# Optimization experiments

Measured on AMD Instinct MI355X. Metric: run time of the kernel, lower is better.

## Reference

```python
import jax, jax.numpy as jnp
import numpy as np
from jax import lax

NUM_POINTS = 1024  # num_points from __init__
BIG = jnp.float32(1e10)


def setup_inputs() -> dict:
    key = jax.random.key(0)
    B, N = 8, 131072
    points = jax.random.normal(key, (B, N, 3), dtype=jnp.float32)
    return {"points": points}


def furthest_point_sampling(points, m):
    """points: [B, N, 3] -> indices [B, m] (int32).
    Standard FPS: start at index 0, iteratively pick the point farthest
    from the current selected set, maintaining a running min-distance.
    """
    B, N, _ = points.shape

    def body(carry, _):
        min_dist, last_idx = carry  # [B, N], [B]
        last_pt = jnp.take_along_axis(points, last_idx[:, None, None], axis=1)  # [B,1,3]
        d = jnp.sum((points - last_pt) ** 2, axis=-1)  # [B, N]
        min_dist = jnp.minimum(min_dist, d)
        nxt = jnp.argmax(min_dist, axis=-1).astype(jnp.int32)  # [B]
        return (min_dist, nxt), nxt

    init_idx = jnp.zeros((B,), dtype=jnp.int32)
    init_dist = jnp.full((B, N), BIG, dtype=points.dtype)
    _, rest = lax.scan(body, (init_dist, init_idx), None, length=m - 1)  # [m-1, B]
    idx = jnp.concatenate([init_idx[None, :], rest], axis=0)  # [m, B]
    return idx.T  # [B, m]


def reference(points):
    idx = furthest_point_sampling(points, NUM_POINTS)            # [B, m]
    xyz1 = jnp.take_along_axis(points, idx[:, :, None], axis=1)  # [B, m, 3]
    return (idx, xyz1)
```

## Files before the change

### kernel.cpp

```cpp
#include <hip/hip_runtime.h>
#include <stdint.h>


#define BATCHES 8
#define NPTS    131072
#define MSEL    1024
#define NBLK    32
#define CHUNK   (NPTS / NBLK)
#define NTH     256
#define PPT     (CHUNK / NTH)
#define NWAVE   (NTH / 64)
#define L2_TIMEOUT_ROUNDS 2000

typedef unsigned int       u32;
typedef unsigned long long u64;
typedef u32 u32x4 __attribute__((ext_vector_type(4)));
typedef u32 u32x2 __attribute__((ext_vector_type(2)));

__device__ __forceinline__ void l2_store_slot(void* p, u32x4 a, u32x2 b) {
    asm volatile("global_store_dwordx4 %0, %1, off sc0\n\t"
                 "global_store_dwordx2 %2, %3, off sc0"
                 :: "v"((u32*)p), "v"(a), "v"(((u32*)p) + 4), "v"(b)
                 : "memory");
}
__device__ __forceinline__ void l2_load_slot(const void* p, u32x4& a, u32x2& b) {
    u32x4 ra; u32x2 rb;
    asm volatile("global_load_dwordx4 %0, %2, off sc0\n\t"
                 "global_load_dwordx2 %1, %3, off sc0\n\t"
                 "s_waitcnt vmcnt(0)"
                 : "=&v"(ra), "=&v"(rb)
                 : "v"((const u32*)p), "v"(((const u32*)p) + 4)
                 : "memory");
    a = ra; b = rb;
}

__global__ __launch_bounds__(NTH, 1) void fps_kernel(
    const float* __restrict__ pts,
    float* __restrict__ out,
    char* __restrict__ l2base,
    u64*  __restrict__ icslots,
    int pad)
{
    __shared__ float lx[CHUNK];
    __shared__ float ly[CHUNK];
    __shared__ float lz[CHUNK];
    __shared__ u64 wkey[NWAVE];
    __shared__ float curs[4];

    const int bid   = blockIdx.x;
    const int b     = bid & (BATCHES - 1);
    const int blk   = bid / BATCHES;
    const int tid   = threadIdx.x;
    const int gbase = blk * CHUNK;
    const float* bp = pts + (size_t)b * NPTS * 3;

    float px[PPT], py[PPT], pz[PPT], md[PPT];
    #pragma unroll
    for (int k = 0; k < PPT; ++k) {
        const int j = k * NTH + tid;
        const size_t gi = (size_t)(gbase + j) * 3;
        px[k] = bp[gi + 0];
        py[k] = bp[gi + 1];
        pz[k] = bp[gi + 2];
        md[k] = 1e10f;
        lx[j] = px[k]; ly[j] = py[k]; lz[j] = pz[k];
    }
    const u32 relt = (u32)(NPTS - 1) - (u32)(gbase + tid);

    float cx = bp[0], cy = bp[1], cz = bp[2];
    if (blk == 0 && tid == 0) {
        out[b * MSEL] = 0.0f;
        float* oxyz = out + BATCHES * MSEL;
        oxyz[(size_t)(b * MSEL) * 3 + 0] = cx;
        oxyz[(size_t)(b * MSEL) * 3 + 1] = cy;
        oxyz[(size_t)(b * MSEL) * 3 + 2] = cz;
    }
    __syncthreads();

    const int wv = tid >> 6;
    const int ln = tid & 63;
    bool useAgent = false;

    for (int s = 1; s < MSEL; ++s) {
        u64 bk = 0ull;
        #pragma unroll
        for (int k = 0; k < PPT; ++k) {
            float dx = __fsub_rn(px[k], cx);
            float dy = __fsub_rn(py[k], cy);
            float dz = __fsub_rn(pz[k], cz);
            float d  = __fadd_rn(__fadd_rn(__fmul_rn(dx, dx), __fmul_rn(dy, dy)),
                                 __fmul_rn(dz, dz));
            float nm = fminf(md[k], d);
            md[k] = nm;
            u64 key = ((u64)__float_as_uint(nm) << 17)
                    | (u64)(relt - (u32)(k * NTH));
            bk = (bk > key) ? bk : key;
        }
        #pragma unroll
        for (int o = 32; o > 0; o >>= 1) {
            u64 t = __shfl_xor(bk, o, 64);
            bk = (bk > t) ? bk : t;
        }
        if (ln == 0) wkey[wv] = bk;
        __syncthreads();

        const u32 tag = (u32)s;
        char* base = l2base + ((size_t)(s & 1) * BATCHES + b) * NBLK * (size_t)pad;
        const size_t icb = ((size_t)(s & 1) * BATCHES + b) * NBLK;

        if (wv == 1 && ln == 0) {
            u64 k0 = wkey[0];
            #pragma unroll
            for (int w = 1; w < NWAVE; ++w) k0 = (k0 > wkey[w]) ? k0 : wkey[w];
            const u64 sv = ((k0 >> 17) << 27) | ((k0 & 0x1FFFFull) << 10) | tag;
            __hip_atomic_store(&icslots[icb + blk], sv,
                               __ATOMIC_RELAXED, __HIP_MEMORY_SCOPE_AGENT);
        }

        if (wv == 0) {
            if (ln == 0) {
                u64 k0 = wkey[0];
                #pragma unroll
                for (int w = 1; w < NWAVE; ++w) k0 = (k0 > wkey[w]) ? k0 : wkey[w];
                const u32 rel = (u32)(k0 & 0x1FFFFull);
                const u32 db  = (u32)(k0 >> 17);
                const int j   = (int)((u32)(NPTS - 1) - rel) - gbase;
                u32x4 a; u32x2 bg;
                a.x = db; a.y = (rel << 10) | tag;
                a.z = __float_as_uint(lx[j]); a.w = __float_as_uint(ly[j]);
                bg.x = __float_as_uint(lz[j]); bg.y = tag;
                l2_store_slot(base + (size_t)blk * pad, a, bg);
            }
            u64 k = 0ull; float x = 0.f, y = 0.f, z = 0.f;
            if (!useAgent) {
                u32x4 A; u32x2 Bv; bool done = false;
                int r = 0;
                for (;;) {
                    if (ln < NBLK && !done) {
                        l2_load_slot(base + (size_t)ln * pad, A, Bv);
                        done = ((A.y & 1023u) == tag) & (Bv.y == tag);
                    }
                    if (__all((ln >= NBLK) | done)) break;
                    if (++r >= L2_TIMEOUT_ROUNDS) { useAgent = true; break; }
                    __builtin_amdgcn_s_sleep(1);
                }
                if (!useAgent && ln < NBLK) {
                    k = ((u64)A.x << 17) | (u64)(A.y >> 10);
                    x = __uint_as_float(A.z);
                    y = __uint_as_float(A.w);
                    z = __uint_as_float(Bv.x);
                }
            }
            if (useAgent) {
                u64 ak = 0ull;
                for (;;) {
                    if (ln < NBLK)
                        ak = __hip_atomic_load(&icslots[icb + ln],
                                               __ATOMIC_RELAXED,
                                               __HIP_MEMORY_SCOPE_AGENT);
                    if (__all((ln >= NBLK) | ((u32)(ak & 1023ull) == tag)))
                        break;
                    __builtin_amdgcn_s_sleep(1);
                }
                #pragma unroll
                for (int o = 16; o > 0; o >>= 1) {
                    u64 t = __shfl_xor(ak, o, 64);
                    ak = (ak > t) ? ak : t;
                }
                const u32 widx = (u32)(NPTS - 1) - (u32)((ak >> 10) & 0x1FFFFull);
                if (ln < 3) {
                    const float v = bp[(size_t)widx * 3 + ln];
                    curs[ln] = v;
                    if (blk == 0)
                        out[BATCHES * MSEL + (size_t)(b * MSEL + s) * 3 + ln] = v;
                }
                if (ln == 0 && blk == 0) out[b * MSEL + s] = (float)widx;
            } else {
                #pragma unroll
                for (int o = 16; o > 0; o >>= 1) {
                    u64 kk = __shfl_xor(k, o, 64);
                    float xx = __shfl_xor(x, o, 64);
                    float yy = __shfl_xor(y, o, 64);
                    float zz = __shfl_xor(z, o, 64);
                    const bool p = kk > k;
                    k = p ? kk : k;
                    x = p ? xx : x;
                    y = p ? yy : y;
                    z = p ? zz : z;
                }
                if (ln == 0) {
                    const u32 widx = (u32)(NPTS - 1) - (u32)(k & 0x1FFFFull);
                    curs[0] = x; curs[1] = y; curs[2] = z;
                    if (blk == 0) {
                        out[b * MSEL + s] = (float)widx;
                        float* oxyz = out + BATCHES * MSEL;
                        oxyz[(size_t)(b * MSEL + s) * 3 + 0] = x;
                        oxyz[(size_t)(b * MSEL + s) * 3 + 1] = y;
                        oxyz[(size_t)(b * MSEL + s) * 3 + 2] = z;
                    }
                }
            }
        }
        __syncthreads();
        cx = curs[0]; cy = curs[1]; cz = curs[2];
    }
}

extern "C" void kernel_launch(void* const* d_in, const int* in_sizes, int n_in,
                              void* d_out, int out_size, void* d_ws, size_t ws_size,
                              hipStream_t stream) {
    const float* pts = (const float*)d_in[0];
    float* out = (float*)d_out;

    const int pad = (ws_size >= (size_t)(2 * BATCHES * NBLK * 128 + 4096))
                        ? 128 : 32;
    char* l2base = (char*)d_ws;
    u64* icslots = (u64*)((char*)d_ws + (size_t)2 * BATCHES * NBLK * pad);

    fps_kernel<<<dim3(BATCHES * NBLK), dim3(NTH), 0, stream>>>(
        pts, out, l2base, icslots, pad);
}
```

Before: 2.249 ms.

## Replace per-block slot polling with atomic max key and arrival counter

Result: slower. 4.664 ms (+107.3%).

```diff
diff --git a/kernel.cpp b/kernel.cpp
--- a/kernel.cpp
+++ b/kernel.cpp
@@ -10,40 +10,19 @@
 #define NTH     256
 #define PPT     (CHUNK / NTH)
 #define NWAVE   (NTH / 64)
-#define L2_TIMEOUT_ROUNDS 2000
+#define L2_TIMEOUT_ROUNDS 4000
 
 typedef unsigned int       u32;
 typedef unsigned long long u64;
 typedef u32 u32x4 __attribute__((ext_vector_type(4)));
-typedef u32 u32x2 __attribute__((ext_vector_type(2)));
-
-__device__ __forceinline__ void l2_store_slot(void* p, u32x4 a, u32x2 b) {
-    asm volatile("global_store_dwordx4 %0, %1, off sc0\n\t"
-                 "global_store_dwordx2 %2, %3, off sc0"
-                 :: "v"((u32*)p), "v"(a), "v"(((u32*)p) + 4), "v"(b)
-                 : "memory");
-}
-__device__ __forceinline__ void l2_load_slot(const void* p, u32x4& a, u32x2& b) {
-    u32x4 ra; u32x2 rb;
-    asm volatile("global_load_dwordx4 %0, %2, off sc0\n\t"
-                 "global_load_dwordx2 %1, %3, off sc0\n\t"
-                 "s_waitcnt vmcnt(0)"
-                 : "=&v"(ra), "=&v"(rb)
-                 : "v"((const u32*)p), "v"(((const u32*)p) + 4)
-                 : "memory");
-    a = ra; b = rb;
-}
 
 __global__ __launch_bounds__(NTH, 1) void fps_kernel(
     const float* __restrict__ pts,
     float* __restrict__ out,
-    char* __restrict__ l2base,
-    u64*  __restrict__ icslots,
+    char* __restrict__ ws,
     int pad)
 {
-    __shared__ float lx[CHUNK];
-    __shared__ float ly[CHUNK];
-    __shared__ float lz[CHUNK];
+    __shared__ float lx[CHUNK], ly[CHUNK], lz[CHUNK];
     __shared__ u64 wkey[NWAVE];
     __shared__ float curs[4];
 
@@ -53,6 +32,11 @@
     const int tid   = threadIdx.x;
     const int gbase = blk * CHUNK;
     const float* bp = pts + (size_t)b * NPTS * 3;
+
+    char* ctl  = ws + (size_t)b * 512;
+    u32*  cntp = (u32*)(ctl + 256);
+    char* plb0 = ws + 4096;
+    u64*  ic   = (u64*)(ws + 4096 + (size_t)2 * BATCHES * NBLK * pad);
 
     float px[PPT], py[PPT], pz[PPT], md[PPT];
     #pragma unroll
@@ -105,91 +89,80 @@
         __syncthreads();
 
         const u32 tag = (u32)s;
-        char* base = l2base + ((size_t)(s & 1) * BATCHES + b) * NBLK * (size_t)pad;
-        const size_t icb = ((size_t)(s & 1) * BATCHES + b) * NBLK;
+        const int par = s & 1;
+        u64*  keyp   = (u64*)(ctl + par * 128);
+        char* plbase = plb0 + ((size_t)(par * BATCHES + b) * NBLK) * pad;
+        const size_t icb = (size_t)(par * BATCHES + b) * NBLK;
 
         if (wv == 1 && ln == 0) {
             u64 k0 = wkey[0];
             #pragma unroll
             for (int w = 1; w < NWAVE; ++w) k0 = (k0 > wkey[w]) ? k0 : wkey[w];
-            const u64 sv = ((k0 >> 17) << 27) | ((k0 & 0x1FFFFull) << 10) | tag;
-            __hip_atomic_store(&icslots[icb + blk], sv,
+            const u32 rel = (u32)(k0 & 0x1FFFFull);
+            const int j = (int)((u32)(NPTS - 1) - rel) - gbase;
+            u32x4 pl;
+            pl.x = __float_as_uint(lx[j]);
+            pl.y = __float_as_uint(ly[j]);
+            pl.z = __float_as_uint(lz[j]);
+            pl.w = tag;
+            const u64 akey = ((u64)tag << 49) | k0;
+            asm volatile(
+                "global_store_dwordx4 %0, %1, off sc0\n\t"
+                "global_atomic_umax_x2 %2, %3, off\n\t"
+                "s_waitcnt vmcnt(0)\n\t"
+                "global_atomic_add %4, %5, off"
+                :: "v"(plbase + (size_t)blk * pad), "v"(pl),
+                   "v"(keyp), "v"(akey),
+                   "v"(cntp), "v"(1u)
+                : "memory");
+            const u64 sv = ((k0 >> 17) << 27) | ((u64)rel << 10) | (u64)tag;
+            __hip_atomic_store(&ic[icb + blk], sv,
                                __ATOMIC_RELAXED, __HIP_MEMORY_SCOPE_AGENT);
         }
 
         if (wv == 0) {
-            if (ln == 0) {
-                u64 k0 = wkey[0];
-                #pragma unroll
-                for (int w = 1; w < NWAVE; ++w) k0 = (k0 > wkey[w]) ? k0 : wkey[w];
-                const u32 rel = (u32)(k0 & 0x1FFFFull);
-                const u32 db  = (u32)(k0 >> 17);
-                const int j   = (int)((u32)(NPTS - 1) - rel) - gbase;
-                u32x4 a; u32x2 bg;
-                a.x = db; a.y = (rel << 10) | tag;
-                a.z = __float_as_uint(lx[j]); a.w = __float_as_uint(ly[j]);
-                bg.x = __float_as_uint(lz[j]); bg.y = tag;
-                l2_store_slot(base + (size_t)blk * pad, a, bg);
+            bool det = false;
+            u32 widx = 0; float x = 0.f, y = 0.f, z = 0.f;
+            if (!useAgent) {
+                const u32 target = 32u * tag;
+                int r = 0; u32 c;
+                for (;;) {
+                    asm volatile("global_load_dword %0, %1, off sc0\n\t"
+                                 "s_waitcnt vmcnt(0)"
+                                 : "=v"(c) : "v"(cntp) : "memory");
+                    if (c >= target) { det = true; break; }
+                    if (++r >= L2_TIMEOUT_ROUNDS) { useAgent = true; break; }
+                    if (r > 16) __builtin_amdgcn_s_sleep(1);
+                }
             }
-            u64 k = 0ull; float x = 0.f, y = 0.f, z = 0.f;
-            if (!useAgent) {
-                u32x4 A; u32x2 Bv; bool done = false;
-                int r = 0;
-                for (;;) {
-                    if (ln < NBLK && !done) {
-                        l2_load_slot(base + (size_t)ln * pad, A, Bv);
-                        done = ((A.y & 1023u) == tag) & (Bv.y == tag);
-                    }
-                    if (__all((ln >= NBLK) | done)) break;
-                    if (++r >= L2_TIMEOUT_ROUNDS) { useAgent = true; break; }
-                    __builtin_amdgcn_s_sleep(1);
-                }
-                if (!useAgent && ln < NBLK) {
-                    k = ((u64)A.x << 17) | (u64)(A.y >> 10);
-                    x = __uint_as_float(A.z);
-                    y = __uint_as_float(A.w);
-                    z = __uint_as_float(Bv.x);
+            if (det) {
+                u64 kf = 0ull; u32x4 PL = {0, 0, 0, 0};
+                if (ln < 32) {
+                    const char* plp = plbase + (size_t)ln * pad;
+                    asm volatile(
+                        "global_load_dwordx2 %0, %2, off sc0\n\t"
+                        "global_load_dwordx4 %1, %3, off sc0\n\t"
+                        "s_waitcnt vmcnt(0)"
+                        : "=&v"(kf), "=&v"(PL)
+                        : "v"(keyp), "v"(plp)
+                        : "memory");
+                }
+                const u32 klo  = (u32)__shfl((int)(u32)kf, 0, 64);
+                const u32 khi  = (u32)__shfl((int)(u32)(kf >> 32), 0, 64);
+                const u32 ktag = khi >> 17;
+                const u32 rel  = klo & 0x1FFFFu;
+                widx = (u32)(NPTS - 1) - rel;
+                const int wblk = (int)(widx >> 12);
+                x = __shfl(__uint_as_float(PL.x), wblk, 64);
+                y = __shfl(__uint_as_float(PL.y), wblk, 64);
+                z = __shfl(__uint_as_float(PL.z), wblk, 64);
+                const u32 wtag = (u32)__shfl((int)PL.w, wblk, 64);
+                if (ktag != tag || wtag != tag) {
+                    det = false; useAgent = true;
                 }
             }
-            if (useAgent) {
-                u64 ak = 0ull;
-                for (;;) {
-                    if (ln < NBLK)
-                        ak = __hip_atomic_load(&icslots[icb + ln],
-                                               __ATOMIC_RELAXED,
-                                               __HIP_MEMORY_SCOPE_AGENT);
-                    if (__all((ln >= NBLK) | ((u32)(ak & 1023ull) == tag)))
-                        break;
-                    __builtin_amdgcn_s_sleep(1);
-                }
-                #pragma unroll
-                for (int o = 16; o > 0; o >>= 1) {
-                    u64 t = __shfl_xor(ak, o, 64);
-                    ak = (ak > t) ? ak : t;
-                }
-                const u32 widx = (u32)(NPTS - 1) - (u32)((ak >> 10) & 0x1FFFFull);
-                if (ln < 3) {
-                    const float v = bp[(size_t)widx * 3 + ln];
-                    curs[ln] = v;
-                    if (blk == 0)
-                        out[BATCHES * MSEL + (size_t)(b * MSEL + s) * 3 + ln] = v;
-                }
-                if (ln == 0 && blk == 0) out[b * MSEL + s] = (float)widx;
-            } else {
-                #pragma unroll
-                for (int o = 16; o > 0; o >>= 1) {
-                    u64 kk = __shfl_xor(k, o, 64);
-                    float xx = __shfl_xor(x, o, 64);
-                    float yy = __shfl_xor(y, o, 64);
-                    float zz = __shfl_xor(z, o, 64);
-                    const bool p = kk > k;
-                    k = p ? kk : k;
-                    x = p ? xx : x;
-                    y = p ? yy : y;
-                    z = p ? zz : z;
-                }
+            if (det) {
                 if (ln == 0) {
-                    const u32 widx = (u32)(NPTS - 1) - (u32)(k & 0x1FFFFull);
                     curs[0] = x; curs[1] = y; curs[2] = z;
                     if (blk == 0) {
                         out[b * MSEL + s] = (float)widx;
@@ -199,6 +172,31 @@
                         oxyz[(size_t)(b * MSEL + s) * 3 + 2] = z;
                     }
                 }
+            } else {
+                u64 ak = 0ull;
+                for (;;) {
+                    if (ln < NBLK)
+                        ak = __hip_atomic_load(&ic[icb + ln], __ATOMIC_RELAXED,
+                                               __HIP_MEMORY_SCOPE_AGENT);
+                    if (__all((ln >= NBLK) | ((u32)(ak & 1023ull) ==
+                                              (tag & 1023u))))
+                        break;
+                    __builtin_amdgcn_s_sleep(1);
+                }
+                #pragma unroll
+                for (int o = 16; o > 0; o >>= 1) {
+                    u64 t = __shfl_xor(ak, o, 64);
+                    ak = (ak > t) ? ak : t;
+                }
+                const u32 fwidx =
+                    (u32)(NPTS - 1) - (u32)((ak >> 10) & 0x1FFFFull);
+                if (ln < 3) {
+                    const float v = bp[(size_t)fwidx * 3 + ln];
+                    curs[ln] = v;
+                    if (blk == 0)
+                        out[BATCHES * MSEL + (size_t)(b * MSEL + s) * 3 + ln] = v;
+                }
+                if (ln == 0 && blk == 0) out[b * MSEL + s] = (float)fwidx;
             }
         }
         __syncthreads();
@@ -212,11 +210,10 @@
     const float* pts = (const float*)d_in[0];
     float* out = (float*)d_out;
 
-    const int pad = (ws_size >= (size_t)(2 * BATCHES * NBLK * 128 + 4096))
+    const int pad = (ws_size >= (size_t)(4096 + 2 * BATCHES * NBLK * 128 + 4096))
                         ? 128 : 32;
-    char* l2base = (char*)d_ws;
-    u64* icslots = (u64*)((char*)d_ws + (size_t)2 * BATCHES * NBLK * pad);
+    hipMemsetAsync(d_ws, 0, 4096, stream);
 
     fps_kernel<<<dim3(BATCHES * NBLK), dim3(NTH), 0, stream>>>(
-        pts, out, l2base, icslots, pad);
+        pts, out, (char*)d_ws, pad);
 }
```

## Speculatively select two FPS points per grid-wide sync round via top-2 reduction

Applied to the files above, without the earlier changes.

Measured after the change: 3.861 ms. 71.6% more time.

```diff
diff --git a/kernel.cpp b/kernel.cpp
--- a/kernel.cpp
+++ b/kernel.cpp
@@ -10,20 +10,28 @@
 #define NTH     256
 #define PPT     (CHUNK / NTH)
 #define NWAVE   (NTH / 64)
-#define L2_TIMEOUT_ROUNDS 2000
+#define L2_TIMEOUT_ROUNDS 4000
 
 typedef unsigned int       u32;
 typedef unsigned long long u64;
 typedef u32 u32x4 __attribute__((ext_vector_type(4)));
 typedef u32 u32x2 __attribute__((ext_vector_type(2)));
 
-__device__ __forceinline__ void l2_store_slot(void* p, u32x4 a, u32x2 b) {
+__device__ __forceinline__ void pmerge(u64& a1, u64& a2, u64 b1, u64 b2) {
+    const u64 lo = (a1 < b1) ? a1 : b1;
+    const u64 hi = (a1 < b1) ? b1 : a1;
+    const u64 m2 = (a2 > b2) ? a2 : b2;
+    a1 = hi;
+    a2 = (lo > m2) ? lo : m2;
+}
+
+__device__ __forceinline__ void st_slot(void* p, u32x4 a, u32x2 b) {
     asm volatile("global_store_dwordx4 %0, %1, off sc0\n\t"
                  "global_store_dwordx2 %2, %3, off sc0"
                  :: "v"((u32*)p), "v"(a), "v"(((u32*)p) + 4), "v"(b)
                  : "memory");
 }
-__device__ __forceinline__ void l2_load_slot(const void* p, u32x4& a, u32x2& b) {
+__device__ __forceinline__ void ld_slot(const void* p, u32x4& a, u32x2& b) {
     u32x4 ra; u32x2 rb;
     asm volatile("global_load_dwordx4 %0, %2, off sc0\n\t"
                  "global_load_dwordx2 %1, %3, off sc0\n\t"
@@ -37,15 +45,12 @@
 __global__ __launch_bounds__(NTH, 1) void fps_kernel(
     const float* __restrict__ pts,
     float* __restrict__ out,
-    char* __restrict__ l2base,
-    u64*  __restrict__ icslots,
+    char* __restrict__ ws,
     int pad)
 {
-    __shared__ float lx[CHUNK];
-    __shared__ float ly[CHUNK];
-    __shared__ float lz[CHUNK];
-    __shared__ u64 wkey[NWAVE];
-    __shared__ float curs[4];
+    __shared__ float lx[CHUNK], ly[CHUNK], lz[CHUNK];
+    __shared__ u64 wkey[NWAVE][2];
+    __shared__ float curs[8];
 
     const int bid   = blockIdx.x;
     const int b     = bid & (BATCHES - 1);
@@ -53,6 +58,9 @@
     const int tid   = threadIdx.x;
     const int gbase = blk * CHUNK;
     const float* bp = pts + (size_t)b * NPTS * 3;
+
+    char* plb0 = ws;
+    u64*  ic   = (u64*)(ws + (size_t)2 * BATCHES * 64 * pad);
 
     float px[PPT], py[PPT], pz[PPT], md[PPT];
     #pragma unroll
@@ -67,142 +75,232 @@
     }
     const u32 relt = (u32)(NPTS - 1) - (u32)(gbase + tid);
 
-    float cx = bp[0], cy = bp[1], cz = bp[2];
+    float c1x = bp[0], c1y = bp[1], c1z = bp[2];
+    float c2x = c1x, c2y = c1y, c2z = c1z;
+    bool have2 = false;
     if (blk == 0 && tid == 0) {
         out[b * MSEL] = 0.0f;
         float* oxyz = out + BATCHES * MSEL;
-        oxyz[(size_t)(b * MSEL) * 3 + 0] = cx;
-        oxyz[(size_t)(b * MSEL) * 3 + 1] = cy;
-        oxyz[(size_t)(b * MSEL) * 3 + 2] = cz;
+        oxyz[(size_t)(b * MSEL) * 3 + 0] = c1x;
+        oxyz[(size_t)(b * MSEL) * 3 + 1] = c1y;
+        oxyz[(size_t)(b * MSEL) * 3 + 2] = c1z;
     }
     __syncthreads();
 
     const int wv = tid >> 6;
     const int ln = tid & 63;
     bool useAgent = false;
-
-    for (int s = 1; s < MSEL; ++s) {
-        u64 bk = 0ull;
-        #pragma unroll
-        for (int k = 0; k < PPT; ++k) {
-            float dx = __fsub_rn(px[k], cx);
-            float dy = __fsub_rn(py[k], cy);
-            float dz = __fsub_rn(pz[k], cz);
-            float d  = __fadd_rn(__fadd_rn(__fmul_rn(dx, dx), __fmul_rn(dy, dy)),
-                                 __fmul_rn(dz, dz));
-            float nm = fminf(md[k], d);
-            md[k] = nm;
-            u64 key = ((u64)__float_as_uint(nm) << 17)
-                    | (u64)(relt - (u32)(k * NTH));
-            bk = (bk > key) ? bk : key;
+    int s = 1;
+
+    for (int rc = 1; s < MSEL; ++rc) {
+        u64 a1 = 0ull, a2 = 0ull;
+        if (have2) {
+            #pragma unroll
+            for (int k = 0; k < PPT; ++k) {
+                float dx = __fsub_rn(px[k], c1x);
+                float dy = __fsub_rn(py[k], c1y);
+                float dz = __fsub_rn(pz[k], c1z);
+                float d1 = __fadd_rn(__fadd_rn(__fmul_rn(dx, dx),
+                                               __fmul_rn(dy, dy)),
+                                     __fmul_rn(dz, dz));
+                float ex = __fsub_rn(px[k], c2x);
+                float ey = __fsub_rn(py[k], c2y);
+                float ez = __fsub_rn(pz[k], c2z);
+                float d2 = __fadd_rn(__fadd_rn(__fmul_rn(ex, ex),
+                                               __fmul_rn(ey, ey)),
+                                     __fmul_rn(ez, ez));
+                float nm = fminf(fminf(md[k], d1), d2);
+                md[k] = nm;
+                u64 key = ((u64)__float_as_uint(nm) << 17)
+                        | (u64)(relt - (u32)(k * NTH));
+                const bool gt = key > a1;
+                const u64 mx2 = (key > a2) ? key : a2;
+                a2 = gt ? a1 : mx2;
+                a1 = gt ? key : a1;
+            }
+        } else {
+            #pragma unroll
+            for (int k = 0; k < PPT; ++k) {
+                float dx = __fsub_rn(px[k], c1x);
+                float dy = __fsub_rn(py[k], c1y);
+                float dz = __fsub_rn(pz[k], c1z);
+                float d1 = __fadd_rn(__fadd_rn(__fmul_rn(dx, dx),
+                                               __fmul_rn(dy, dy)),
+                                     __fmul_rn(dz, dz));
+                float nm = fminf(md[k], d1);
+                md[k] = nm;
+                u64 key = ((u64)__float_as_uint(nm) << 17)
+                        | (u64)(relt - (u32)(k * NTH));
+                const bool gt = key > a1;
+                const u64 mx2 = (key > a2) ? key : a2;
+                a2 = gt ? a1 : mx2;
+                a1 = gt ? key : a1;
+            }
         }
         #pragma unroll
         for (int o = 32; o > 0; o >>= 1) {
-            u64 t = __shfl_xor(bk, o, 64);
-            bk = (bk > t) ? bk : t;
+            u64 b1 = __shfl_xor(a1, o, 64);
+            u64 b2 = __shfl_xor(a2, o, 64);
+            pmerge(a1, a2, b1, b2);
         }
-        if (ln == 0) wkey[wv] = bk;
+        if (ln == 0) { wkey[wv][0] = a1; wkey[wv][1] = a2; }
         __syncthreads();
 
-        const u32 tag = (u32)s;
-        char* base = l2base + ((size_t)(s & 1) * BATCHES + b) * NBLK * (size_t)pad;
-        const size_t icb = ((size_t)(s & 1) * BATCHES + b) * NBLK;
+        const u32 tag = (u32)rc;
+        const int par = rc & 1;
+        char* plbase = plb0 + ((size_t)(par * BATCHES + b) * 64) * pad;
+        const size_t icb = (size_t)(par * BATCHES + b) * 64;
 
         if (wv == 1 && ln == 0) {
-            u64 k0 = wkey[0];
+            u64 k1 = wkey[0][0], k2 = wkey[0][1];
             #pragma unroll
-            for (int w = 1; w < NWAVE; ++w) k0 = (k0 > wkey[w]) ? k0 : wkey[w];
-            const u64 sv = ((k0 >> 17) << 27) | ((k0 & 0x1FFFFull) << 10) | tag;
-            __hip_atomic_store(&icslots[icb + blk], sv,
+            for (int w = 1; w < NWAVE; ++w) pmerge(k1, k2, wkey[w][0], wkey[w][1]);
+            const u32 rel1 = (u32)(k1 & 0x1FFFFull);
+            const u32 rel2 = (u32)(k2 & 0x1FFFFull);
+            const int j1 = (int)((u32)(NPTS - 1) - rel1) - gbase;
+            const int j2 = (int)((u32)(NPTS - 1) - rel2) - gbase;
+            u32x4 A; u32x2 Bv;
+            A.x = (u32)(k1 >> 17); A.y = (rel1 << 10) | tag;
+            A.z = __float_as_uint(lx[j1]); A.w = __float_as_uint(ly[j1]);
+            Bv.x = __float_as_uint(lz[j1]); Bv.y = tag;
+            st_slot(plbase + (size_t)blk * pad, A, Bv);
+            A.x = (u32)(k2 >> 17); A.y = (rel2 << 10) | tag;
+            A.z = __float_as_uint(lx[j2]); A.w = __float_as_uint(ly[j2]);
+            Bv.x = __float_as_uint(lz[j2]); Bv.y = tag;
+            st_slot(plbase + (size_t)(32 + blk) * pad, A, Bv);
+            __hip_atomic_store(&ic[icb + 2 * blk],
+                               ((k1 >> 17) << 27) | ((u64)rel1 << 10) | tag,
+                               __ATOMIC_RELAXED, __HIP_MEMORY_SCOPE_AGENT);
+            __hip_atomic_store(&ic[icb + 2 * blk + 1],
+                               ((k2 >> 17) << 27) | ((u64)rel2 << 10) | tag,
                                __ATOMIC_RELAXED, __HIP_MEMORY_SCOPE_AGENT);
         }
 
         if (wv == 0) {
-            if (ln == 0) {
-                u64 k0 = wkey[0];
-                #pragma unroll
-                for (int w = 1; w < NWAVE; ++w) k0 = (k0 > wkey[w]) ? k0 : wkey[w];
-                const u32 rel = (u32)(k0 & 0x1FFFFull);
-                const u32 db  = (u32)(k0 >> 17);
-                const int j   = (int)((u32)(NPTS - 1) - rel) - gbase;
-                u32x4 a; u32x2 bg;
-                a.x = db; a.y = (rel << 10) | tag;
-                a.z = __float_as_uint(lx[j]); a.w = __float_as_uint(ly[j]);
-                bg.x = __float_as_uint(lz[j]); bg.y = tag;
-                l2_store_slot(base + (size_t)blk * pad, a, bg);
-            }
-            u64 k = 0ull; float x = 0.f, y = 0.f, z = 0.f;
+            u32x4 LA = {0, 0, 0, 0}; u32x2 LB = {0, 0};
+            bool done = false;
             if (!useAgent) {
-                u32x4 A; u32x2 Bv; bool done = false;
+                const char* myp = plbase + (size_t)ln * pad;
                 int r = 0;
                 for (;;) {
-                    if (ln < NBLK && !done) {
-                        l2_load_slot(base + (size_t)ln * pad, A, Bv);
-                        done = ((A.y & 1023u) == tag) & (Bv.y == tag);
+                    if (!done) {
+                        u32x4 ta; u32x2 tb;
+                        ld_slot(myp, ta, tb);
+                        if (((ta.y & 1023u) == tag) & (tb.y == tag)) {
+                            LA = ta; LB = tb; done = true;
+                        }
                     }
-                    if (__all((ln >= NBLK) | done)) break;
+                    if (__all(done)) break;
                     if (++r >= L2_TIMEOUT_ROUNDS) { useAgent = true; break; }
+                    if (r > 16) __builtin_amdgcn_s_sleep(1);
+                }
+            }
+            if (!useAgent) {
+                u64 k1 = ((u64)LA.x << 17) | (u64)(LA.y >> 10);
+                u64 k2 = 0ull;
+                #pragma unroll
+                for (int o = 32; o > 0; o >>= 1) {
+                    u64 b1 = __shfl_xor(k1, o, 64);
+                    u64 b2 = __shfl_xor(k2, o, 64);
+                    pmerge(k1, k2, b1, b2);
+                }
+                const u32 rel1  = (u32)(k1 & 0x1FFFFull);
+                const u32 rel2  = (u32)(k2 & 0x1FFFFull);
+                const u32 widx1 = (u32)(NPTS - 1) - rel1;
+                const u32 widx2 = (u32)(NPTS - 1) - rel2;
+                const int wb1   = (int)(widx1 >> 12);
+                const int wbb   = (int)(widx2 >> 12);
+                const int src2  = (wbb == wb1) ? (32 + wb1) : wbb;
+                const float x1 = __shfl(__uint_as_float(LA.z), wb1, 64);
+                const float y1 = __shfl(__uint_as_float(LA.w), wb1, 64);
+                const float z1 = __shfl(__uint_as_float(LB.x), wb1, 64);
+                const float x2 = __shfl(__uint_as_float(LA.z), src2, 64);
+                const float y2 = __shfl(__uint_as_float(LA.w), src2, 64);
+                const float z2 = __shfl(__uint_as_float(LB.x), src2, 64);
+                const float ddx = __fsub_rn(x2, x1);
+                const float ddy = __fsub_rn(y2, y1);
+                const float ddz = __fsub_rn(z2, z1);
+                const float dd  = __fadd_rn(__fadd_rn(__fmul_rn(ddx, ddx),
+                                                      __fmul_rn(ddy, ddy)),
+                                            __fmul_rn(ddz, ddz));
+                const bool spec = (__float_as_uint(dd) >= (u32)(k2 >> 17))
+                                  && (s + 1 < MSEL);
+                if (ln == 0) {
+                    curs[0] = x1; curs[1] = y1; curs[2] = z1;
+                    curs[3] = x2; curs[4] = y2; curs[5] = z2;
+                    curs[6] = spec ? 1.0f : 0.0f;
+                    if (blk == 0) {
+                        out[b * MSEL + s] = (float)widx1;
+                        float* oxyz = out + BATCHES * MSEL;
+                        oxyz[(size_t)(b * MSEL + s) * 3 + 0] = x1;
+                        oxyz[(size_t)(b * MSEL + s) * 3 + 1] = y1;
+                        oxyz[(size_t)(b * MSEL + s) * 3 + 2] = z1;
+                        if (spec) {
+                            out[b * MSEL + s + 1] = (float)widx2;
+                            oxyz[(size_t)(b * MSEL + s + 1) * 3 + 0] = x2;
+                            oxyz[(size_t)(b * MSEL + s + 1) * 3 + 1] = y2;
+                            oxyz[(size_t)(b * MSEL + s + 1) * 3 + 2] = z2;
+                        }
+                    }
+                }
+            } else {
+                const int ii = (ln < 32) ? (2 * ln) : (2 * (ln - 32) + 1);
+                u64 sv = 0ull;
+                for (;;) {
+                    sv = __hip_atomic_load(&ic[icb + ii], __ATOMIC_RELAXED,
+                                           __HIP_MEMORY_SCOPE_AGENT);
+                    if (__all((u32)(sv & 1023ull) == (tag & 1023u))) break;
                     __builtin_amdgcn_s_sleep(1);
                 }
-                if (!useAgent && ln < NBLK) {
-                    k = ((u64)A.x << 17) | (u64)(A.y >> 10);
-                    x = __uint_as_float(A.z);
-                    y = __uint_as_float(A.w);
-                    z = __uint_as_float(Bv.x);
-                }
-            }
-            if (useAgent) {
-                u64 ak = 0ull;
-                for (;;) {
-                    if (ln < NBLK)
-                        ak = __hip_atomic_load(&icslots[icb + ln],
-                                               __ATOMIC_RELAXED,
-                                               __HIP_MEMORY_SCOPE_AGENT);
-                    if (__all((ln >= NBLK) | ((u32)(ak & 1023ull) == tag)))
-                        break;
-                    __builtin_amdgcn_s_sleep(1);
-                }
+                u64 k1 = ((sv >> 27) << 17) | ((sv >> 10) & 0x1FFFFull);
+                u64 k2 = 0ull;
                 #pragma unroll
-                for (int o = 16; o > 0; o >>= 1) {
-                    u64 t = __shfl_xor(ak, o, 64);
-                    ak = (ak > t) ? ak : t;
-                }
-                const u32 widx = (u32)(NPTS - 1) - (u32)((ak >> 10) & 0x1FFFFull);
-                if (ln < 3) {
-                    const float v = bp[(size_t)widx * 3 + ln];
-                    curs[ln] = v;
-                    if (blk == 0)
-                        out[BATCHES * MSEL + (size_t)(b * MSEL + s) * 3 + ln] = v;
-                }
-                if (ln == 0 && blk == 0) out[b * MSEL + s] = (float)widx;
-            } else {
-                #pragma unroll
-                for (int o = 16; o > 0; o >>= 1) {
-                    u64 kk = __shfl_xor(k, o, 64);
-                    float xx = __shfl_xor(x, o, 64);
-                    float yy = __shfl_xor(y, o, 64);
-                    float zz = __shfl_xor(z, o, 64);
-                    const bool p = kk > k;
-                    k = p ? kk : k;
-                    x = p ? xx : x;
-                    y = p ? yy : y;
-                    z = p ? zz : z;
-                }
+                for (int o = 32; o > 0; o >>= 1) {
+                    u64 b1 = __shfl_xor(k1, o, 64);
+                    u64 b2 = __shfl_xor(k2, o, 64);
+                    pmerge(k1, k2, b1, b2);
+                }
+                const u32 widx1 = (u32)(NPTS - 1) - (u32)(k1 & 0x1FFFFull);
+                const u32 widx2 = (u32)(NPTS - 1) - (u32)(k2 & 0x1FFFFull);
                 if (ln == 0) {
-                    const u32 widx = (u32)(NPTS - 1) - (u32)(k & 0x1FFFFull);
-                    curs[0] = x; curs[1] = y; curs[2] = z;
+                    const float x1 = bp[(size_t)widx1 * 3 + 0];
+                    const float y1 = bp[(size_t)widx1 * 3 + 1];
+                    const float z1 = bp[(size_t)widx1 * 3 + 2];
+                    const float x2 = bp[(size_t)widx2 * 3 + 0];
+                    const float y2 = bp[(size_t)widx2 * 3 + 1];
+                    const float z2 = bp[(size_t)widx2 * 3 + 2];
+                    const float ddx = __fsub_rn(x2, x1);
+                    const float ddy = __fsub_rn(y2, y1);
+                    const float ddz = __fsub_rn(z2, z1);
+                    const float dd  = __fadd_rn(__fadd_rn(__fmul_rn(ddx, ddx),
+                                                          __fmul_rn(ddy, ddy)),
+                                                __fmul_rn(ddz, ddz));
+                    const bool spec = (__float_as_uint(dd) >= (u32)(k2 >> 17))
+                                      && (s + 1 < MSEL);
+                    curs[0] = x1; curs[1] = y1; curs[2] = z1;
+                    curs[3] = x2; curs[4] = y2; curs[5] = z2;
+                    curs[6] = spec ? 1.0f : 0.0f;
                     if (blk == 0) {
-                        out[b * MSEL + s] = (float)widx;
+                        out[b * MSEL + s] = (float)widx1;
                         float* oxyz = out + BATCHES * MSEL;
-                        oxyz[(size_t)(b * MSEL + s) * 3 + 0] = x;
-                        oxyz[(size_t)(b * MSEL + s) * 3 + 1] = y;
-                        oxyz[(size_t)(b * MSEL + s) * 3 + 2] = z;
+                        oxyz[(size_t)(b * MSEL + s) * 3 + 0] = x1;
+                        oxyz[(size_t)(b * MSEL + s) * 3 + 1] = y1;
+                        oxyz[(size_t)(b * MSEL + s) * 3 + 2] = z1;
+                        if (spec) {
+                            out[b * MSEL + s + 1] = (float)widx2;
+                            oxyz[(size_t)(b * MSEL + s + 1) * 3 + 0] = x2;
+                            oxyz[(size_t)(b * MSEL + s + 1) * 3 + 1] = y2;
+                            oxyz[(size_t)(b * MSEL + s + 1) * 3 + 2] = z2;
+                        }
                     }
                 }
             }
         }
         __syncthreads();
-        cx = curs[0]; cy = curs[1]; cz = curs[2];
+        c1x = curs[0]; c1y = curs[1]; c1z = curs[2];
+        c2x = curs[3]; c2y = curs[4]; c2z = curs[5];
+        have2 = (curs[6] != 0.0f);
+        s += 1 + (have2 ? 1 : 0);
     }
 }
 
@@ -212,11 +310,10 @@
     const float* pts = (const float*)d_in[0];
     float* out = (float*)d_out;
 
-    const int pad = (ws_size >= (size_t)(2 * BATCHES * NBLK * 128 + 4096))
-                        ? 128 : 32;
-    char* l2base = (char*)d_ws;
-    u64* icslots = (u64*)((char*)d_ws + (size_t)2 * BATCHES * NBLK * pad);
+    int pad = 32;
+    if (ws_size >= (size_t)(2 * BATCHES * 64 * 128 + 8192 + 1024)) pad = 128;
+    else if (ws_size >= (size_t)(2 * BATCHES * 64 * 64 + 8192 + 1024)) pad = 64;
 
     fps_kernel<<<dim3(BATCHES * NBLK), dim3(NTH), 0, stream>>>(
-        pts, out, l2base, icslots, pad);
-}
+        pts, out, (char*)d_ws, pad);
+}
```
